# Optimization experiments

Hardware: AMD Instinct MI355X
Metric: run time of the kernel (lower is better)

Reference implementation:

```python
import jax, jax.numpy as jnp
import numpy as np

CUTOFF = 5.0       # module __init__ arg
BOX_L = 40.0       # side of cubic region positions are drawn from (OBC: no box passed)
N_ATOMS = 8192
MAX_PAIRS = 1_048_576  # static bound on directed pairs (expected ~550k)


def setup_inputs() -> dict:
    key = jax.random.key(0)
    positions = jax.random.uniform(key, (N_ATOMS, 3), dtype=jnp.float32) * BOX_L
    return {"positions": positions}


def _pairwise_dist(x):
    # Euclidean distance matrix via the gram trick (avoids [N,N,3] intermediate).
    sq = jnp.sum(x * x, axis=1)
    d2 = sq[:, None] + sq[None, :] - 2.0 * (x @ x.T)
    return jnp.sqrt(jnp.maximum(d2, 0.0))


def _safe_norm(dr):
    # norm with zero-safe gradient (padded pairs have dr == 0)
    d2 = jnp.sum(dr * dr, axis=1)
    ok = d2 > 0
    return jnp.where(ok, jnp.sqrt(jnp.where(ok, d2, 1.0)), 0.0)


def reference(positions):
    n = positions.shape[0]
    dist = _pairwise_dist(positions)                      # [N, N]
    mask = (dist < CUTOFF) & (~jnp.eye(n, dtype=bool))    # exclude self-pairs
    # torch.argwhere equivalent, padded to static size; padding -> (0, 0)
    i, j = jnp.nonzero(mask, size=MAX_PAIRS, fill_value=0)
    pairs = jnp.stack([i, j], axis=1).astype(jnp.int32)   # [MAX_PAIRS, 2]
    # pairs_buffer_scales: 1 where i < j else 0 (padding (0,0) -> 0)
    buffer_scales = (i < j).astype(jnp.int32)
    # pairs_ds (pbc_flag=False): ||r_j - r_i||
    dr = positions[j] - positions[i]                      # [MAX_PAIRS, 3]
    ds = _safe_norm(dr)
    return pairs, buffer_scales, ds
```

## Files before the change

### kernel.cpp

```cpp
#include <hip/hip_runtime.h>

#define MAXP 1048576
#define NATOMS 8192
#define D2_CUT 0x1.8ffffep+4f
#define CINV 0.175f
#define CAP 192

#define W_SORTPOS 0
#define W_SORTID  32768
#define W_ROWCNT  36864
#define W_ROWOFF  45056
#define W_CELLOFF 53248
#define W_CELLCNT 53760
#define W_CELLCUR 54272

__device__ __forceinline__ float sq3_nc(float x, float y, float z) {
#pragma clang fp contract(off)
  float a = x * x;
  float b = y * y;
  float c = z * z;
  return (a + b) + c;
}

__device__ __forceinline__ float d2_gram(float xi, float yi, float zi, float sqi,
                                         float xj, float yj, float zj, float sqj) {
#pragma clang fp contract(off)
  float g = xi * xj;
  g = __builtin_fmaf(yi, yj, g);
  g = __builtin_fmaf(zi, zj, g);
  float t = sqi + sqj;
  float d2 = t - 2.0f * g;
  return d2;
}

__device__ __forceinline__ float d2_direct(float xi, float yi, float zi,
                                           float xj, float yj, float zj) {
#pragma clang fp contract(off)
  float dx = xj - xi;
  float dy = yj - yi;
  float dz = zj - zi;
  float a = dx * dx;
  float b = dy * dy;
  float c = dz * dz;
  return (a + b) + c;
}

__device__ __forceinline__ int cellco(float v) {
  int c = (int)(v * CINV);
  return c < 0 ? 0 : (c > 6 ? 6 : c);
}

__global__ __launch_bounds__(256) void nl_pack(float* __restrict__ out,
                                               float* __restrict__ ws) {
  const int gtid = blockIdx.x * 256 + threadIdx.x;
  float4* o4 = (float4*)out;
#pragma unroll
  for (int k = 0; k < 16; ++k)
    o4[k * 65536 + gtid] = make_float4(0.f, 0.f, 0.f, 0.f);
  if (gtid < 512) ((int*)(ws + W_CELLCNT))[gtid] = 0;
}

__global__ __launch_bounds__(256) void nl_cellcount(const float* __restrict__ pos,
                                                    float* __restrict__ ws) {
  const int a = blockIdx.x * 256 + threadIdx.x;
  float x = pos[3 * a], y = pos[3 * a + 1], z = pos[3 * a + 2];
  int cl = cellco(x) + 7 * cellco(y) + 49 * cellco(z);
  atomicAdd(&((int*)(ws + W_CELLCNT))[cl], 1);
}

__global__ __launch_bounds__(512) void nl_cellscan(float* __restrict__ ws) {
  const int* cellcnt = (const int*)(ws + W_CELLCNT);
  int* celloff = (int*)(ws + W_CELLOFF);
  int* cellcur = (int*)(ws + W_CELLCUR);
  __shared__ int s[512];
  const int tid = threadIdx.x;
  s[tid] = (tid < 343) ? cellcnt[tid] : 0;
  __syncthreads();
  for (int off = 1; off < 512; off <<= 1) {
    int v = (tid >= off) ? s[tid - off] : 0;
    __syncthreads();
    s[tid] += v;
    __syncthreads();
  }
  if (tid < 344) celloff[tid] = (tid == 0) ? 0 : s[tid - 1];
  cellcur[tid] = 0;
}

__global__ __launch_bounds__(256) void nl_scatter(const float* __restrict__ pos,
                                                  float* __restrict__ ws) {
  const int a = blockIdx.x * 256 + threadIdx.x;
  float x = pos[3 * a], y = pos[3 * a + 1], z = pos[3 * a + 2];
  int cl = cellco(x) + 7 * cellco(y) + 49 * cellco(z);
  int slot = ((const int*)(ws + W_CELLOFF))[cl] +
             atomicAdd(&((int*)(ws + W_CELLCUR))[cl], 1);
  ((float4*)(ws + W_SORTPOS))[slot] = make_float4(x, y, z, sq3_nc(x, y, z));
  ((unsigned short*)(ws + W_SORTID))[slot] = (unsigned short)a;
}

__global__ __launch_bounds__(256, 4) void nl_count(const float* __restrict__ pos,
                                                   float* __restrict__ ws) {
  const int lane = threadIdx.x & 63;
  const int wave = threadIdx.x >> 6;
  const int row = blockIdx.x * 4 + wave;

  const float4* __restrict__ sp4 = (const float4*)(ws + W_SORTPOS);
  const int* __restrict__ celloff = (const int*)(ws + W_CELLOFF);
  int* rowcnt = (int*)(ws + W_ROWCNT);

  const float xi = pos[3 * row], yi = pos[3 * row + 1], zi = pos[3 * row + 2];
  const float sqi = sq3_nc(xi, yi, zi);
  int cx = cellco(xi), cy = cellco(yi), cz = cellco(zi);
  int x0 = max(cx - 1, 0), x1 = min(cx + 1, 6);
  int y0 = max(cy - 1, 0), y1 = min(cy + 1, 6);
  int z0 = max(cz - 1, 0), z1 = min(cz + 1, 6);

  int cnt = 0;
  for (int icz = z0; icz <= z1; ++icz)
    for (int icy = y0; icy <= y1; ++icy) {
      int cb = 7 * icy + 49 * icz;
      int st = celloff[cb + x0];
      int en = celloff[cb + x1 + 1];
      for (int bb = st; bb < en; bb += 64) {
        int t = bb + lane;
        bool v = t < en;
        int t2 = v ? t : (en - 1);
        float4 p = sp4[t2];
        float d2 = d2_gram(xi, yi, zi, sqi, p.x, p.y, p.z, p.w);
        cnt += (v && d2 < D2_CUT) ? 1 : 0;
      }
    }
  for (int off = 32; off > 0; off >>= 1) cnt += __shfl_down(cnt, off, 64);
  if (lane == 0) rowcnt[row] = cnt - 1;
}

__global__ __launch_bounds__(1024) void nl_rowscan(float* __restrict__ ws) {
  const int* cnts = (const int*)(ws + W_ROWCNT);
  int* offs = (int*)(ws + W_ROWOFF);
  __shared__ int s[1024];
  const int tid = threadIdx.x;
  const int base = tid * 8;
  int local[8];
  int sum = 0;
#pragma unroll
  for (int k = 0; k < 8; ++k) { local[k] = sum; sum += cnts[base + k]; }
  s[tid] = sum;
  __syncthreads();
  for (int off = 1; off < 1024; off <<= 1) {
    int v = (tid >= off) ? s[tid - off] : 0;
    __syncthreads();
    s[tid] += v;
    __syncthreads();
  }
  int excl = (tid == 0) ? 0 : s[tid - 1];
#pragma unroll
  for (int k = 0; k < 8; ++k) offs[base + k] = excl + local[k];
}

__global__ __launch_bounds__(256, 4) void nl_write(const float* __restrict__ pos,
                                                   float* __restrict__ out,
                                                   const float* __restrict__ ws) {
  __shared__ unsigned int bmap[4][256];
  __shared__ unsigned short stj[4][CAP];
  const int lane = threadIdx.x & 63;
  const int wave = threadIdx.x >> 6;
  const int row = blockIdx.x * 4 + wave;

  const float4* __restrict__ sp4 = (const float4*)(ws + W_SORTPOS);
  const unsigned short* __restrict__ sid = (const unsigned short*)(ws + W_SORTID);
  const int* __restrict__ celloff = (const int*)(ws + W_CELLOFF);
  const int* __restrict__ rowoff = (const int*)(ws + W_ROWOFF);

#pragma unroll
  for (int q = 0; q < 4; ++q) bmap[wave][lane + 64 * q] = 0u;

  const float xi = pos[3 * row], yi = pos[3 * row + 1], zi = pos[3 * row + 2];
  const float sqi = sq3_nc(xi, yi, zi);
  int cx = cellco(xi), cy = cellco(yi), cz = cellco(zi);
  int x0 = max(cx - 1, 0), x1 = min(cx + 1, 6);
  int y0 = max(cy - 1, 0), y1 = min(cy + 1, 6);
  int z0 = max(cz - 1, 0), z1 = min(cz + 1, 6);

  for (int icz = z0; icz <= z1; ++icz)
    for (int icy = y0; icy <= y1; ++icy) {
      int cb = 7 * icy + 49 * icz;
      int st = celloff[cb + x0];
      int en = celloff[cb + x1 + 1];
      for (int bb = st; bb < en; bb += 64) {
        int t = bb + lane;
        bool v = t < en;
        int t2 = v ? t : (en - 1);
        float4 p = sp4[t2];
        int jd = sid[t2];
        float d2 = d2_gram(xi, yi, zi, sqi, p.x, p.y, p.z, p.w);
        if (v && d2 < D2_CUT)
          atomicOr(&bmap[wave][jd >> 5], 1u << (jd & 31));
      }
    }
  if (lane == 0)
    atomicAnd(&bmap[wave][row >> 5], ~(1u << (row & 31)));

  int ktot = 0;
#pragma unroll
  for (int seg = 0; seg < 4; ++seg) {
    int w = seg * 64 + lane;
    unsigned bits = bmap[wave][w];
    int pc = __popc(bits);
    int incl = pc;
    for (int d = 1; d < 64; d <<= 1) {
      int u = __shfl_up(incl, d, 64);
      if (lane >= d) incl += u;
    }
    int base = ktot + incl - pc;
    while (bits) {
      int b = __builtin_ctz(bits);
      bits &= bits - 1;
      if (base < CAP) stj[wave][base] = (unsigned short)(w * 32 + b);
      ++base;
    }
    ktot += __shfl(incl, 63, 64);
  }

  int k = ktot > CAP ? CAP : ktot;
  int ro = rowoff[row];
  for (int s = lane; s < k; s += 64) {
    int j = stj[wave][s];
    int o = ro + s;
    if ((unsigned)o < MAXP) {
      float xj = pos[3 * j], yj = pos[3 * j + 1], zj = pos[3 * j + 2];
      float ds = sqrtf(d2_direct(xi, yi, zi, xj, yj, zj));
      ((float2*)out)[o] = make_float2((float)row, (float)j);
      out[2 * MAXP + o] = (row < j) ? 1.0f : 0.0f;
      out[3 * MAXP + o] = ds;
    }
  }
}

extern "C" void kernel_launch(void* const* d_in, const int* in_sizes, int n_in,
                              void* d_out, int out_size, void* d_ws, size_t ws_size,
                              hipStream_t stream) {
  const float* pos = (const float*)d_in[0];
  float* out = (float*)d_out;
  float* ws = (float*)d_ws;

  nl_pack<<<256, 256, 0, stream>>>(out, ws);
  nl_cellcount<<<32, 256, 0, stream>>>(pos, ws);
  nl_cellscan<<<1, 512, 0, stream>>>(ws);
  nl_scatter<<<32, 256, 0, stream>>>(pos, ws);
  nl_count<<<2048, 256, 0, stream>>>(pos, ws);
  nl_rowscan<<<1, 1024, 0, stream>>>(ws);
  nl_write<<<2048, 256, 0, stream>>>(pos, out, ws);
}
```

Before: 96.04 us.

## Process one cell per block, staging neighbor-cell positions in shared memory

Count and write kernels now launch one 512-thread block per spatial cell instead of one wave per atom row. Each block loads the 27-cell neighborhood's positions (and ids) into LDS once, then eight waves reuse them for every atom in the cell. This cuts redundant global loads of neighbor data. In exchange, only 343 blocks are launched, which can underuse a GPU with many CUs. Empty or heavily populated cells can also unbalance the work, and neighborhoods larger than the LDS capacity fall back to slower global lookups.

```diff
diff --git a/kernel.cpp b/kernel.cpp
--- a/kernel.cpp
+++ b/kernel.cpp
@@ -5,6 +5,7 @@
 #define D2_CUT 0x1.8ffffep+4f
 #define CINV 0.175f
 #define CAP 192
+#define CAPL 1024
 
 #define W_SORTPOS 0
 #define W_SORTID  32768
@@ -97,40 +98,67 @@
   ((unsigned short*)(ws + W_SORTID))[slot] = (unsigned short)a;
 }
 
-__global__ __launch_bounds__(256, 4) void nl_count(const float* __restrict__ pos,
-                                                   float* __restrict__ ws) {
-  const int lane = threadIdx.x & 63;
-  const int wave = threadIdx.x >> 6;
-  const int row = blockIdx.x * 4 + wave;
-
+__global__ __launch_bounds__(512, 4) void nl_count(float* __restrict__ ws) {
+  __shared__ float4 cp[CAPL];
+  __shared__ int sg[9], scum[10];
+  const int tid = threadIdx.x;
+  const int lane = tid & 63;
+  const int wave = tid >> 6;
+  const int c = blockIdx.x;
+
+  const int* __restrict__ celloff = (const int*)(ws + W_CELLOFF);
   const float4* __restrict__ sp4 = (const float4*)(ws + W_SORTPOS);
-  const int* __restrict__ celloff = (const int*)(ws + W_CELLOFF);
+  const unsigned short* __restrict__ sid = (const unsigned short*)(ws + W_SORTID);
   int* rowcnt = (int*)(ws + W_ROWCNT);
 
-  const float xi = pos[3 * row], yi = pos[3 * row + 1], zi = pos[3 * row + 2];
-  const float sqi = sq3_nc(xi, yi, zi);
-  int cx = cellco(xi), cy = cellco(yi), cz = cellco(zi);
-  int x0 = max(cx - 1, 0), x1 = min(cx + 1, 6);
-  int y0 = max(cy - 1, 0), y1 = min(cy + 1, 6);
-  int z0 = max(cz - 1, 0), z1 = min(cz + 1, 6);
-
-  int cnt = 0;
-  for (int icz = z0; icz <= z1; ++icz)
-    for (int icy = y0; icy <= y1; ++icy) {
-      int cb = 7 * icy + 49 * icz;
-      int st = celloff[cb + x0];
-      int en = celloff[cb + x1 + 1];
-      for (int bb = st; bb < en; bb += 64) {
-        int t = bb + lane;
-        bool v = t < en;
-        int t2 = v ? t : (en - 1);
-        float4 p = sp4[t2];
-        float d2 = d2_gram(xi, yi, zi, sqi, p.x, p.y, p.z, p.w);
-        cnt += (v && d2 < D2_CUT) ? 1 : 0;
-      }
+  const int rs = celloff[c], re = celloff[c + 1];
+  if (rs == re) return;
+
+  if (tid == 0) {
+    int ccx = c % 7, ccy = (c / 7) % 7, ccz = c / 49;
+    int x0 = ccx > 0 ? ccx - 1 : 0, x1 = ccx < 6 ? ccx + 1 : 6;
+    int y0 = ccy > 0 ? ccy - 1 : 0, y1 = ccy < 6 ? ccy + 1 : 6;
+    int z0 = ccz > 0 ? ccz - 1 : 0, z1 = ccz < 6 ? ccz + 1 : 6;
+    int ns = 0, cum = 0;
+    for (int icz = z0; icz <= z1; ++icz)
+      for (int icy = y0; icy <= y1; ++icy) {
+        int cb = 7 * icy + 49 * icz;
+        int st = celloff[cb + x0], en = celloff[cb + x1 + 1];
+        sg[ns] = st; scum[ns] = cum; cum += en - st; ++ns;
+      }
+    for (; ns < 9; ++ns) { sg[ns] = 0; scum[ns] = cum; }
+    scum[9] = cum;
+  }
+  __syncthreads();
+
+  const int T = scum[9];
+  for (int st = 0; st < 9; ++st) {
+    int cs = scum[st], len = scum[st + 1] - cs;
+    for (int i = tid; i < len; i += 512)
+      if (cs + i < CAPL) cp[cs + i] = sp4[sg[st] + i];
+  }
+  __syncthreads();
+
+  for (int sl = rs + wave; sl < re; sl += 8) {
+    float4 pi = sp4[sl];
+    int cnt = 0;
+    for (int bb = 0; bb < T; bb += 64) {
+      int idx = bb + lane;
+      bool v = idx < T;
+      int i2 = v ? idx : T - 1;
+      float4 p;
+      if (i2 < CAPL) p = cp[i2];
+      else {
+        int ss = 0;
+        while (scum[ss + 1] <= i2) ++ss;
+        p = sp4[sg[ss] + (i2 - scum[ss])];
+      }
+      float d2 = d2_gram(pi.x, pi.y, pi.z, pi.w, p.x, p.y, p.z, p.w);
+      cnt += (v && d2 < D2_CUT) ? 1 : 0;
     }
-  for (int off = 32; off > 0; off >>= 1) cnt += __shfl_down(cnt, off, 64);
-  if (lane == 0) rowcnt[row] = cnt - 1;
+    for (int off = 32; off > 0; off >>= 1) cnt += __shfl_down(cnt, off, 64);
+    if (lane == 0) rowcnt[sid[sl]] = cnt - 1;
+  }
 }
 
 __global__ __launch_bounds__(1024) void nl_rowscan(float* __restrict__ ws) {
@@ -156,81 +184,113 @@
   for (int k = 0; k < 8; ++k) offs[base + k] = excl + local[k];
 }
 
-__global__ __launch_bounds__(256, 4) void nl_write(const float* __restrict__ pos,
+__global__ __launch_bounds__(512, 4) void nl_write(const float* __restrict__ pos,
                                                    float* __restrict__ out,
                                                    const float* __restrict__ ws) {
-  __shared__ unsigned int bmap[4][256];
-  __shared__ unsigned short stj[4][CAP];
-  const int lane = threadIdx.x & 63;
-  const int wave = threadIdx.x >> 6;
-  const int row = blockIdx.x * 4 + wave;
-
+  __shared__ float4 cp[CAPL];
+  __shared__ unsigned short cid[CAPL];
+  __shared__ unsigned int bmap[8][256];
+  __shared__ unsigned short stj[8][CAP];
+  __shared__ int sg[9], scum[10];
+  const int tid = threadIdx.x;
+  const int lane = tid & 63;
+  const int wave = tid >> 6;
+  const int c = blockIdx.x;
+
+  const int* __restrict__ celloff = (const int*)(ws + W_CELLOFF);
   const float4* __restrict__ sp4 = (const float4*)(ws + W_SORTPOS);
   const unsigned short* __restrict__ sid = (const unsigned short*)(ws + W_SORTID);
-  const int* __restrict__ celloff = (const int*)(ws + W_CELLOFF);
   const int* __restrict__ rowoff = (const int*)(ws + W_ROWOFF);
 
-#pragma unroll
-  for (int q = 0; q < 4; ++q) bmap[wave][lane + 64 * q] = 0u;
-
-  const float xi = pos[3 * row], yi = pos[3 * row + 1], zi = pos[3 * row + 2];
-  const float sqi = sq3_nc(xi, yi, zi);
-  int cx = cellco(xi), cy = cellco(yi), cz = cellco(zi);
-  int x0 = max(cx - 1, 0), x1 = min(cx + 1, 6);
-  int y0 = max(cy - 1, 0), y1 = min(cy + 1, 6);
-  int z0 = max(cz - 1, 0), z1 = min(cz + 1, 6);
-
-  for (int icz = z0; icz <= z1; ++icz)
-    for (int icy = y0; icy <= y1; ++icy) {
-      int cb = 7 * icy + 49 * icz;
-      int st = celloff[cb + x0];
-      int en = celloff[cb + x1 + 1];
-      for (int bb = st; bb < en; bb += 64) {
-        int t = bb + lane;
-        bool v = t < en;
-        int t2 = v ? t : (en - 1);
-        float4 p = sp4[t2];
-        int jd = sid[t2];
-        float d2 = d2_gram(xi, yi, zi, sqi, p.x, p.y, p.z, p.w);
-        if (v && d2 < D2_CUT)
-          atomicOr(&bmap[wave][jd >> 5], 1u << (jd & 31));
-      }
+  const int rs = celloff[c], re = celloff[c + 1];
+  if (rs == re) return;
+
+  if (tid == 0) {
+    int ccx = c % 7, ccy = (c / 7) % 7, ccz = c / 49;
+    int x0 = ccx > 0 ? ccx - 1 : 0, x1 = ccx < 6 ? ccx + 1 : 6;
+    int y0 = ccy > 0 ? ccy - 1 : 0, y1 = ccy < 6 ? ccy + 1 : 6;
+    int z0 = ccz > 0 ? ccz - 1 : 0, z1 = ccz < 6 ? ccz + 1 : 6;
+    int ns = 0, cum = 0;
+    for (int icz = z0; icz <= z1; ++icz)
+      for (int icy = y0; icy <= y1; ++icy) {
+        int cb = 7 * icy + 49 * icz;
+        int st = celloff[cb + x0], en = celloff[cb + x1 + 1];
+        sg[ns] = st; scum[ns] = cum; cum += en - st; ++ns;
+      }
+    for (; ns < 9; ++ns) { sg[ns] = 0; scum[ns] = cum; }
+    scum[9] = cum;
+  }
+  __syncthreads();
+
+  const int T = scum[9];
+  for (int st = 0; st < 9; ++st) {
+    int cs = scum[st], len = scum[st + 1] - cs;
+    for (int i = tid; i < len; i += 512)
+      if (cs + i < CAPL) {
+        cp[cs + i] = sp4[sg[st] + i];
+        cid[cs + i] = sid[sg[st] + i];
+      }
+  }
+  __syncthreads();
+
+  for (int sl = rs + wave; sl < re; sl += 8) {
+#pragma unroll
+    for (int q = 0; q < 4; ++q) bmap[wave][lane + 64 * q] = 0u;
+    float4 pi = sp4[sl];
+    const int rid = sid[sl];
+
+    for (int bb = 0; bb < T; bb += 64) {
+      int idx = bb + lane;
+      bool v = idx < T;
+      int i2 = v ? idx : T - 1;
+      float4 p; int jd;
+      if (i2 < CAPL) { p = cp[i2]; jd = cid[i2]; }
+      else {
+        int ss = 0;
+        while (scum[ss + 1] <= i2) ++ss;
+        int gidx = sg[ss] + (i2 - scum[ss]);
+        p = sp4[gidx]; jd = sid[gidx];
+      }
+      float d2 = d2_gram(pi.x, pi.y, pi.z, pi.w, p.x, p.y, p.z, p.w);
+      if (v && d2 < D2_CUT)
+        atomicOr(&bmap[wave][jd >> 5], 1u << (jd & 31));
     }
-  if (lane == 0)
-    atomicAnd(&bmap[wave][row >> 5], ~(1u << (row & 31)));
-
-  int ktot = 0;
-#pragma unroll
-  for (int seg = 0; seg < 4; ++seg) {
-    int w = seg * 64 + lane;
-    unsigned bits = bmap[wave][w];
-    int pc = __popc(bits);
-    int incl = pc;
-    for (int d = 1; d < 64; d <<= 1) {
-      int u = __shfl_up(incl, d, 64);
-      if (lane >= d) incl += u;
+    if (lane == 0)
+      atomicAnd(&bmap[wave][rid >> 5], ~(1u << (rid & 31)));
+
+    int ktot = 0;
+#pragma unroll
+    for (int seg = 0; seg < 4; ++seg) {
+      int w = seg * 64 + lane;
+      unsigned bits = bmap[wave][w];
+      int pc = __popc(bits);
+      int incl = pc;
+      for (int d = 1; d < 64; d <<= 1) {
+        int u = __shfl_up(incl, d, 64);
+        if (lane >= d) incl += u;
+      }
+      int bpos = ktot + incl - pc;
+      while (bits) {
+        int b = __builtin_ctz(bits);
+        bits &= bits - 1;
+        if (bpos < CAP) stj[wave][bpos] = (unsigned short)(w * 32 + b);
+        ++bpos;
+      }
+      ktot += __shfl(incl, 63, 64);
     }
-    int base = ktot + incl - pc;
-    while (bits) {
-      int b = __builtin_ctz(bits);
-      bits &= bits - 1;
-      if (base < CAP) stj[wave][base] = (unsigned short)(w * 32 + b);
-      ++base;
-    }
-    ktot += __shfl(incl, 63, 64);
-  }
-
-  int k = ktot > CAP ? CAP : ktot;
-  int ro = rowoff[row];
-  for (int s = lane; s < k; s += 64) {
-    int j = stj[wave][s];
-    int o = ro + s;
-    if ((unsigned)o < MAXP) {
-      float xj = pos[3 * j], yj = pos[3 * j + 1], zj = pos[3 * j + 2];
-      float ds = sqrtf(d2_direct(xi, yi, zi, xj, yj, zj));
-      ((float2*)out)[o] = make_float2((float)row, (float)j);
-      out[2 * MAXP + o] = (row < j) ? 1.0f : 0.0f;
-      out[3 * MAXP + o] = ds;
+
+    int k = ktot > CAP ? CAP : ktot;
+    int ro = rowoff[rid];
+    for (int s2 = lane; s2 < k; s2 += 64) {
+      int j = stj[wave][s2];
+      int o = ro + s2;
+      if ((unsigned)o < MAXP) {
+        float xj = pos[3 * j], yj = pos[3 * j + 1], zj = pos[3 * j + 2];
+        float ds = sqrtf(d2_direct(pi.x, pi.y, pi.z, xj, yj, zj));
+        ((float2*)out)[o] = make_float2((float)rid, (float)j);
+        out[2 * MAXP + o] = (rid < j) ? 1.0f : 0.0f;
+        out[3 * MAXP + o] = ds;
+      }
     }
   }
 }
@@ -246,7 +306,7 @@
   nl_cellcount<<<32, 256, 0, stream>>>(pos, ws);
   nl_cellscan<<<1, 512, 0, stream>>>(ws);
   nl_scatter<<<32, 256, 0, stream>>>(pos, ws);
-  nl_count<<<2048, 256, 0, stream>>>(pos, ws);
+  nl_count<<<343, 512, 0, stream>>>(ws);
   nl_rowscan<<<1, 1024, 0, stream>>>(ws);
-  nl_write<<<2048, 256, 0, stream>>>(pos, out, ws);
-}
+  nl_write<<<343, 512, 0, stream>>>(pos, out, ws);
+}
```

Measured after the change: 112.1 us. 16.7% more time.

## Fuse cell binning into one block and process rows in cell-sorted order

Applied to the files above, without the earlier changes.

Merges the cell count, cell scan and scatter kernels into a single one-block kernel that uses shared-memory histograms, removing two launches and the global atomics. The count and write kernels now assign waves to rows in cell-sorted slot order, so neighbouring waves scan the same cells and reuse cached data, and they read the row position from the sorted buffer. Occupancy hints rise to 8 blocks per CU. In exchange, binning runs on a single block, which serialises that work.

```diff
diff --git a/kernel.cpp b/kernel.cpp
--- a/kernel.cpp
+++ b/kernel.cpp
@@ -11,8 +11,6 @@
 #define W_ROWCNT  36864
 #define W_ROWOFF  45056
 #define W_CELLOFF 53248
-#define W_CELLCNT 53760
-#define W_CELLCUR 54272
 
 __device__ __forceinline__ float sq3_nc(float x, float y, float z) {
 #pragma clang fp contract(off)
@@ -50,66 +48,70 @@
   return c < 0 ? 0 : (c > 6 ? 6 : c);
 }
 
-__global__ __launch_bounds__(256) void nl_pack(float* __restrict__ out,
-                                               float* __restrict__ ws) {
+__global__ __launch_bounds__(256) void nl_pack(float* __restrict__ out) {
   const int gtid = blockIdx.x * 256 + threadIdx.x;
   float4* o4 = (float4*)out;
 #pragma unroll
   for (int k = 0; k < 16; ++k)
     o4[k * 65536 + gtid] = make_float4(0.f, 0.f, 0.f, 0.f);
-  if (gtid < 512) ((int*)(ws + W_CELLCNT))[gtid] = 0;
-}
-
-__global__ __launch_bounds__(256) void nl_cellcount(const float* __restrict__ pos,
-                                                    float* __restrict__ ws) {
-  const int a = blockIdx.x * 256 + threadIdx.x;
-  float x = pos[3 * a], y = pos[3 * a + 1], z = pos[3 * a + 2];
-  int cl = cellco(x) + 7 * cellco(y) + 49 * cellco(z);
-  atomicAdd(&((int*)(ws + W_CELLCNT))[cl], 1);
-}
-
-__global__ __launch_bounds__(512) void nl_cellscan(float* __restrict__ ws) {
-  const int* cellcnt = (const int*)(ws + W_CELLCNT);
-  int* celloff = (int*)(ws + W_CELLOFF);
-  int* cellcur = (int*)(ws + W_CELLCUR);
+}
+
+__global__ __launch_bounds__(1024) void nl_prep(const float* __restrict__ pos,
+                                                float* __restrict__ ws) {
+  __shared__ int hcnt[343];
+  __shared__ int hoff[344];
+  __shared__ int hcur[343];
   __shared__ int s[512];
   const int tid = threadIdx.x;
-  s[tid] = (tid < 343) ? cellcnt[tid] : 0;
+  if (tid < 343) { hcnt[tid] = 0; hcur[tid] = 0; }
+  __syncthreads();
+
+  float x[8], y[8], z[8];
+  int cl[8];
+#pragma unroll
+  for (int k = 0; k < 8; ++k) {
+    int a = tid + k * 1024;
+    x[k] = pos[3 * a]; y[k] = pos[3 * a + 1]; z[k] = pos[3 * a + 2];
+    cl[k] = cellco(x[k]) + 7 * cellco(y[k]) + 49 * cellco(z[k]);
+    atomicAdd(&hcnt[cl[k]], 1);
+  }
+  __syncthreads();
+
+  if (tid < 512) s[tid] = (tid < 343) ? hcnt[tid] : 0;
   __syncthreads();
   for (int off = 1; off < 512; off <<= 1) {
-    int v = (tid >= off) ? s[tid - off] : 0;
-    __syncthreads();
-    s[tid] += v;
-    __syncthreads();
-  }
-  if (tid < 344) celloff[tid] = (tid == 0) ? 0 : s[tid - 1];
-  cellcur[tid] = 0;
-}
-
-__global__ __launch_bounds__(256) void nl_scatter(const float* __restrict__ pos,
-                                                  float* __restrict__ ws) {
-  const int a = blockIdx.x * 256 + threadIdx.x;
-  float x = pos[3 * a], y = pos[3 * a + 1], z = pos[3 * a + 2];
-  int cl = cellco(x) + 7 * cellco(y) + 49 * cellco(z);
-  int slot = ((const int*)(ws + W_CELLOFF))[cl] +
-             atomicAdd(&((int*)(ws + W_CELLCUR))[cl], 1);
-  ((float4*)(ws + W_SORTPOS))[slot] = make_float4(x, y, z, sq3_nc(x, y, z));
-  ((unsigned short*)(ws + W_SORTID))[slot] = (unsigned short)a;
-}
-
-__global__ __launch_bounds__(256, 4) void nl_count(const float* __restrict__ pos,
-                                                   float* __restrict__ ws) {
+    int v = (tid < 512 && tid >= off) ? s[tid - off] : 0;
+    __syncthreads();
+    if (tid < 512) s[tid] += v;
+    __syncthreads();
+  }
+  if (tid < 343) hoff[tid] = (tid == 0) ? 0 : s[tid - 1];
+  if (tid == 343) hoff[343] = NATOMS;
+  __syncthreads();
+  if (tid < 344) ((int*)(ws + W_CELLOFF))[tid] = hoff[tid];
+
+  unsigned short* sortid = (unsigned short*)(ws + W_SORTID);
+  float4* sortpos = (float4*)(ws + W_SORTPOS);
+#pragma unroll
+  for (int k = 0; k < 8; ++k) {
+    int slot = hoff[cl[k]] + atomicAdd(&hcur[cl[k]], 1);
+    sortid[slot] = (unsigned short)(tid + k * 1024);
+    sortpos[slot] = make_float4(x[k], y[k], z[k], sq3_nc(x[k], y[k], z[k]));
+  }
+}
+
+__global__ __launch_bounds__(256, 8) void nl_count(float* __restrict__ ws) {
   const int lane = threadIdx.x & 63;
   const int wave = threadIdx.x >> 6;
-  const int row = blockIdx.x * 4 + wave;
+  const int slot = blockIdx.x * 4 + wave;
 
   const float4* __restrict__ sp4 = (const float4*)(ws + W_SORTPOS);
+  const unsigned short* __restrict__ sid = (const unsigned short*)(ws + W_SORTID);
   const int* __restrict__ celloff = (const int*)(ws + W_CELLOFF);
   int* rowcnt = (int*)(ws + W_ROWCNT);
 
-  const float xi = pos[3 * row], yi = pos[3 * row + 1], zi = pos[3 * row + 2];
-  const float sqi = sq3_nc(xi, yi, zi);
-  int cx = cellco(xi), cy = cellco(yi), cz = cellco(zi);
+  const float4 pi = sp4[slot];
+  int cx = cellco(pi.x), cy = cellco(pi.y), cz = cellco(pi.z);
   int x0 = max(cx - 1, 0), x1 = min(cx + 1, 6);
   int y0 = max(cy - 1, 0), y1 = min(cy + 1, 6);
   int z0 = max(cz - 1, 0), z1 = min(cz + 1, 6);
@@ -125,12 +127,12 @@
         bool v = t < en;
         int t2 = v ? t : (en - 1);
         float4 p = sp4[t2];
-        float d2 = d2_gram(xi, yi, zi, sqi, p.x, p.y, p.z, p.w);
+        float d2 = d2_gram(pi.x, pi.y, pi.z, pi.w, p.x, p.y, p.z, p.w);
         cnt += (v && d2 < D2_CUT) ? 1 : 0;
       }
     }
   for (int off = 32; off > 0; off >>= 1) cnt += __shfl_down(cnt, off, 64);
-  if (lane == 0) rowcnt[row] = cnt - 1;
+  if (lane == 0) rowcnt[sid[slot]] = cnt - 1;
 }
 
 __global__ __launch_bounds__(1024) void nl_rowscan(float* __restrict__ ws) {
@@ -156,14 +158,14 @@
   for (int k = 0; k < 8; ++k) offs[base + k] = excl + local[k];
 }
 
-__global__ __launch_bounds__(256, 4) void nl_write(const float* __restrict__ pos,
+__global__ __launch_bounds__(256, 8) void nl_write(const float* __restrict__ pos,
                                                    float* __restrict__ out,
                                                    const float* __restrict__ ws) {
   __shared__ unsigned int bmap[4][256];
   __shared__ unsigned short stj[4][CAP];
   const int lane = threadIdx.x & 63;
   const int wave = threadIdx.x >> 6;
-  const int row = blockIdx.x * 4 + wave;
+  const int slot = blockIdx.x * 4 + wave;
 
   const float4* __restrict__ sp4 = (const float4*)(ws + W_SORTPOS);
   const unsigned short* __restrict__ sid = (const unsigned short*)(ws + W_SORTID);
@@ -173,9 +175,9 @@
 #pragma unroll
   for (int q = 0; q < 4; ++q) bmap[wave][lane + 64 * q] = 0u;
 
-  const float xi = pos[3 * row], yi = pos[3 * row + 1], zi = pos[3 * row + 2];
-  const float sqi = sq3_nc(xi, yi, zi);
-  int cx = cellco(xi), cy = cellco(yi), cz = cellco(zi);
+  const float4 pi = sp4[slot];
+  const int rid = sid[slot];
+  int cx = cellco(pi.x), cy = cellco(pi.y), cz = cellco(pi.z);
   int x0 = max(cx - 1, 0), x1 = min(cx + 1, 6);
   int y0 = max(cy - 1, 0), y1 = min(cy + 1, 6);
   int z0 = max(cz - 1, 0), z1 = min(cz + 1, 6);
@@ -191,13 +193,13 @@
         int t2 = v ? t : (en - 1);
         float4 p = sp4[t2];
         int jd = sid[t2];
-        float d2 = d2_gram(xi, yi, zi, sqi, p.x, p.y, p.z, p.w);
+        float d2 = d2_gram(pi.x, pi.y, pi.z, pi.w, p.x, p.y, p.z, p.w);
         if (v && d2 < D2_CUT)
           atomicOr(&bmap[wave][jd >> 5], 1u << (jd & 31));
       }
     }
   if (lane == 0)
-    atomicAnd(&bmap[wave][row >> 5], ~(1u << (row & 31)));
+    atomicAnd(&bmap[wave][rid >> 5], ~(1u << (rid & 31)));
 
   int ktot = 0;
 #pragma unroll
@@ -210,26 +212,26 @@
       int u = __shfl_up(incl, d, 64);
       if (lane >= d) incl += u;
     }
-    int base = ktot + incl - pc;
+    int bpos = ktot + incl - pc;
     while (bits) {
       int b = __builtin_ctz(bits);
       bits &= bits - 1;
-      if (base < CAP) stj[wave][base] = (unsigned short)(w * 32 + b);
-      ++base;
+      if (bpos < CAP) stj[wave][bpos] = (unsigned short)(w * 32 + b);
+      ++bpos;
     }
     ktot += __shfl(incl, 63, 64);
   }
 
   int k = ktot > CAP ? CAP : ktot;
-  int ro = rowoff[row];
-  for (int s = lane; s < k; s += 64) {
-    int j = stj[wave][s];
-    int o = ro + s;
+  int ro = rowoff[rid];
+  for (int s2 = lane; s2 < k; s2 += 64) {
+    int j = stj[wave][s2];
+    int o = ro + s2;
     if ((unsigned)o < MAXP) {
       float xj = pos[3 * j], yj = pos[3 * j + 1], zj = pos[3 * j + 2];
-      float ds = sqrtf(d2_direct(xi, yi, zi, xj, yj, zj));
-      ((float2*)out)[o] = make_float2((float)row, (float)j);
-      out[2 * MAXP + o] = (row < j) ? 1.0f : 0.0f;
+      float ds = sqrtf(d2_direct(pi.x, pi.y, pi.z, xj, yj, zj));
+      ((float2*)out)[o] = make_float2((float)rid, (float)j);
+      out[2 * MAXP + o] = (rid < j) ? 1.0f : 0.0f;
       out[3 * MAXP + o] = ds;
     }
   }
@@ -242,11 +244,9 @@
   float* out = (float*)d_out;
   float* ws = (float*)d_ws;
 
-  nl_pack<<<256, 256, 0, stream>>>(out, ws);
-  nl_cellcount<<<32, 256, 0, stream>>>(pos, ws);
-  nl_cellscan<<<1, 512, 0, stream>>>(ws);
-  nl_scatter<<<32, 256, 0, stream>>>(pos, ws);
-  nl_count<<<2048, 256, 0, stream>>>(pos, ws);
+  nl_pack<<<256, 256, 0, stream>>>(out);
+  nl_prep<<<1, 1024, 0, stream>>>(pos, ws);
+  nl_count<<<2048, 256, 0, stream>>>(ws);
   nl_rowscan<<<1, 1024, 0, stream>>>(ws);
   nl_write<<<2048, 256, 0, stream>>>(pos, out, ws);
 }
```

Result: no change. 96.66 us (+0.6%).

## Process rows in cell-sorted order and skip out-of-range neighbor cell rows

Applied to the files above, without the earlier changes.

Each wave now takes its query atom from the cell-sorted position array instead of the original order, so neighbouring waves scan the same cells and get better cache reuse. Whole z slabs and y rows of the 3x3x3 stencil are skipped when their bounding slab is farther than the cutoff, using a small safety margin. Launch bounds raise the occupancy hint to 8 blocks, and the cellcur reset moves into the pack kernel. The margin-based skip could drop pairs if it is set too tight.

```diff
diff --git a/kernel.cpp b/kernel.cpp
--- a/kernel.cpp
+++ b/kernel.cpp
@@ -4,6 +4,8 @@
 #define NATOMS 8192
 #define D2_CUT 0x1.8ffffep+4f
 #define CINV 0.175f
+#define CELLW 5.7142857f
+#define SKIP2 25.03f
 #define CAP 192
 
 #define W_SORTPOS 0
@@ -50,6 +52,12 @@
   return c < 0 ? 0 : (c > 6 ? 6 : c);
 }
 
+__device__ __forceinline__ float slabdist(float v, int ic) {
+  float lo = ic * CELLW - 0.02f;
+  float hi = (ic + 1) * CELLW + 0.02f;
+  return fmaxf(0.0f, fmaxf(lo - v, v - hi));
+}
+
 __global__ __launch_bounds__(256) void nl_pack(float* __restrict__ out,
                                                float* __restrict__ ws) {
   const int gtid = blockIdx.x * 256 + threadIdx.x;
@@ -57,7 +65,7 @@
 #pragma unroll
   for (int k = 0; k < 16; ++k)
     o4[k * 65536 + gtid] = make_float4(0.f, 0.f, 0.f, 0.f);
-  if (gtid < 512) ((int*)(ws + W_CELLCNT))[gtid] = 0;
+  if (gtid < 1024) ((int*)(ws + W_CELLCNT))[gtid] = 0;
 }
 
 __global__ __launch_bounds__(256) void nl_cellcount(const float* __restrict__ pos,
@@ -71,7 +79,6 @@
 __global__ __launch_bounds__(512) void nl_cellscan(float* __restrict__ ws) {
   const int* cellcnt = (const int*)(ws + W_CELLCNT);
   int* celloff = (int*)(ws + W_CELLOFF);
-  int* cellcur = (int*)(ws + W_CELLCUR);
   __shared__ int s[512];
   const int tid = threadIdx.x;
   s[tid] = (tid < 343) ? cellcnt[tid] : 0;
@@ -83,7 +90,6 @@
     __syncthreads();
   }
   if (tid < 344) celloff[tid] = (tid == 0) ? 0 : s[tid - 1];
-  cellcur[tid] = 0;
 }
 
 __global__ __launch_bounds__(256) void nl_scatter(const float* __restrict__ pos,
@@ -97,26 +103,30 @@
   ((unsigned short*)(ws + W_SORTID))[slot] = (unsigned short)a;
 }
 
-__global__ __launch_bounds__(256, 4) void nl_count(const float* __restrict__ pos,
-                                                   float* __restrict__ ws) {
+__global__ __launch_bounds__(256, 8) void nl_count(float* __restrict__ ws) {
   const int lane = threadIdx.x & 63;
   const int wave = threadIdx.x >> 6;
-  const int row = blockIdx.x * 4 + wave;
+  const int slot = blockIdx.x * 4 + wave;
 
   const float4* __restrict__ sp4 = (const float4*)(ws + W_SORTPOS);
+  const unsigned short* __restrict__ sid = (const unsigned short*)(ws + W_SORTID);
   const int* __restrict__ celloff = (const int*)(ws + W_CELLOFF);
   int* rowcnt = (int*)(ws + W_ROWCNT);
 
-  const float xi = pos[3 * row], yi = pos[3 * row + 1], zi = pos[3 * row + 2];
-  const float sqi = sq3_nc(xi, yi, zi);
-  int cx = cellco(xi), cy = cellco(yi), cz = cellco(zi);
+  const float4 pi = sp4[slot];
+  int cx = cellco(pi.x), cy = cellco(pi.y), cz = cellco(pi.z);
   int x0 = max(cx - 1, 0), x1 = min(cx + 1, 6);
   int y0 = max(cy - 1, 0), y1 = min(cy + 1, 6);
   int z0 = max(cz - 1, 0), z1 = min(cz + 1, 6);
 
   int cnt = 0;
-  for (int icz = z0; icz <= z1; ++icz)
+  for (int icz = z0; icz <= z1; ++icz) {
+    float dz = slabdist(pi.z, icz);
+    float dz2 = dz * dz;
+    if (dz2 > SKIP2) continue;
     for (int icy = y0; icy <= y1; ++icy) {
+      float dy = slabdist(pi.y, icy);
+      if (dz2 + dy * dy > SKIP2) continue;
       int cb = 7 * icy + 49 * icz;
       int st = celloff[cb + x0];
       int en = celloff[cb + x1 + 1];
@@ -125,12 +135,13 @@
         bool v = t < en;
         int t2 = v ? t : (en - 1);
         float4 p = sp4[t2];
-        float d2 = d2_gram(xi, yi, zi, sqi, p.x, p.y, p.z, p.w);
+        float d2 = d2_gram(pi.x, pi.y, pi.z, pi.w, p.x, p.y, p.z, p.w);
         cnt += (v && d2 < D2_CUT) ? 1 : 0;
       }
     }
+  }
   for (int off = 32; off > 0; off >>= 1) cnt += __shfl_down(cnt, off, 64);
-  if (lane == 0) rowcnt[row] = cnt - 1;
+  if (lane == 0) rowcnt[sid[slot]] = cnt - 1;
 }
 
 __global__ __launch_bounds__(1024) void nl_rowscan(float* __restrict__ ws) {
@@ -156,14 +167,14 @@
   for (int k = 0; k < 8; ++k) offs[base + k] = excl + local[k];
 }
 
-__global__ __launch_bounds__(256, 4) void nl_write(const float* __restrict__ pos,
+__global__ __launch_bounds__(256, 8) void nl_write(const float* __restrict__ pos,
                                                    float* __restrict__ out,
                                                    const float* __restrict__ ws) {
   __shared__ unsigned int bmap[4][256];
   __shared__ unsigned short stj[4][CAP];
   const int lane = threadIdx.x & 63;
   const int wave = threadIdx.x >> 6;
-  const int row = blockIdx.x * 4 + wave;
+  const int slot = blockIdx.x * 4 + wave;
 
   const float4* __restrict__ sp4 = (const float4*)(ws + W_SORTPOS);
   const unsigned short* __restrict__ sid = (const unsigned short*)(ws + W_SORTID);
@@ -173,15 +184,20 @@
 #pragma unroll
   for (int q = 0; q < 4; ++q) bmap[wave][lane + 64 * q] = 0u;
 
-  const float xi = pos[3 * row], yi = pos[3 * row + 1], zi = pos[3 * row + 2];
-  const float sqi = sq3_nc(xi, yi, zi);
-  int cx = cellco(xi), cy = cellco(yi), cz = cellco(zi);
+  const float4 pi = sp4[slot];
+  const int rid = sid[slot];
+  int cx = cellco(pi.x), cy = cellco(pi.y), cz = cellco(pi.z);
   int x0 = max(cx - 1, 0), x1 = min(cx + 1, 6);
   int y0 = max(cy - 1, 0), y1 = min(cy + 1, 6);
   int z0 = max(cz - 1, 0), z1 = min(cz + 1, 6);
 
-  for (int icz = z0; icz <= z1; ++icz)
+  for (int icz = z0; icz <= z1; ++icz) {
+    float dz = slabdist(pi.z, icz);
+    float dz2 = dz * dz;
+    if (dz2 > SKIP2) continue;
     for (int icy = y0; icy <= y1; ++icy) {
+      float dy = slabdist(pi.y, icy);
+      if (dz2 + dy * dy > SKIP2) continue;
       int cb = 7 * icy + 49 * icz;
       int st = celloff[cb + x0];
       int en = celloff[cb + x1 + 1];
@@ -191,13 +207,14 @@
         int t2 = v ? t : (en - 1);
         float4 p = sp4[t2];
         int jd = sid[t2];
-        float d2 = d2_gram(xi, yi, zi, sqi, p.x, p.y, p.z, p.w);
+        float d2 = d2_gram(pi.x, pi.y, pi.z, pi.w, p.x, p.y, p.z, p.w);
         if (v && d2 < D2_CUT)
           atomicOr(&bmap[wave][jd >> 5], 1u << (jd & 31));
       }
     }
+  }
   if (lane == 0)
-    atomicAnd(&bmap[wave][row >> 5], ~(1u << (row & 31)));
+    atomicAnd(&bmap[wave][rid >> 5], ~(1u << (rid & 31)));
 
   int ktot = 0;
 #pragma unroll
@@ -210,26 +227,26 @@
       int u = __shfl_up(incl, d, 64);
       if (lane >= d) incl += u;
     }
-    int base = ktot + incl - pc;
+    int bpos = ktot + incl - pc;
     while (bits) {
       int b = __builtin_ctz(bits);
       bits &= bits - 1;
-      if (base < CAP) stj[wave][base] = (unsigned short)(w * 32 + b);
-      ++base;
+      if (bpos < CAP) stj[wave][bpos] = (unsigned short)(w * 32 + b);
+      ++bpos;
     }
     ktot += __shfl(incl, 63, 64);
   }
 
   int k = ktot > CAP ? CAP : ktot;
-  int ro = rowoff[row];
-  for (int s = lane; s < k; s += 64) {
-    int j = stj[wave][s];
-    int o = ro + s;
+  int ro = rowoff[rid];
+  for (int s2 = lane; s2 < k; s2 += 64) {
+    int j = stj[wave][s2];
+    int o = ro + s2;
     if ((unsigned)o < MAXP) {
       float xj = pos[3 * j], yj = pos[3 * j + 1], zj = pos[3 * j + 2];
-      float ds = sqrtf(d2_direct(xi, yi, zi, xj, yj, zj));
-      ((float2*)out)[o] = make_float2((float)row, (float)j);
-      out[2 * MAXP + o] = (row < j) ? 1.0f : 0.0f;
+      float ds = sqrtf(d2_direct(pi.x, pi.y, pi.z, xj, yj, zj));
+      ((float2*)out)[o] = make_float2((float)rid, (float)j);
+      out[2 * MAXP + o] = (rid < j) ? 1.0f : 0.0f;
       out[3 * MAXP + o] = ds;
     }
   }
@@ -246,7 +263,7 @@
   nl_cellcount<<<32, 256, 0, stream>>>(pos, ws);
   nl_cellscan<<<1, 512, 0, stream>>>(ws);
   nl_scatter<<<32, 256, 0, stream>>>(pos, ws);
-  nl_count<<<2048, 256, 0, stream>>>(pos, ws);
+  nl_count<<<2048, 256, 0, stream>>>(ws);
   nl_rowscan<<<1, 1024, 0, stream>>>(ws);
   nl_write<<<2048, 256, 0, stream>>>(pos, out, ws);
 }
```

Result: no change. 96.74 us (+0.7%).
